# Kernel optimization log

Hardware: AMD Instinct MI355X
Metric: run time of the kernel (lower is better)

The kernel has to match this reference:

```python
import jax, jax.numpy as jnp
import numpy as np

NUM_DOTS = 100
IMG_SIZE = 4096


def setup_inputs() -> dict:
    key = jax.random.key(0)
    k1, k2, k3, k4 = jax.random.split(key, 4)
    adv_patch = jax.random.uniform(k1, (3, IMG_SIZE, IMG_SIZE), dtype=jnp.float32)
    centers = jax.random.uniform(k2, (NUM_DOTS, 2), dtype=jnp.float32)
    radii = jax.random.uniform(k3, (NUM_DOTS,), dtype=jnp.float32)
    colors = jax.random.uniform(k4, (NUM_DOTS, 3), dtype=jnp.float32)
    return {"adv_patch": adv_patch, "centers": centers, "radii": radii, "colors": colors}


def reference(adv_patch, centers, radii, colors):
    # Replicates PatchTrainer.forward: for each dot, draw a filled circle
    # (PIL ellipse with center (int(cx*S), int(cy*S)) and radius int(r*S/5))
    # and overwrite the three channels with the dot's color inside the circle.
    # Later dots overwrite earlier ones (sequential masked_fill_), so we scan.
    S = adv_patch.shape[-1]
    # int() truncation on non-negative values == floor
    xc = jnp.floor(centers[:, 0] * S)          # [N] horizontal center (image x)
    yc = jnp.floor(centers[:, 1] * S)          # [N] vertical center (image y)
    r = jnp.floor(radii * (S / 5.0))           # [N]
    xs = jnp.arange(S, dtype=adv_patch.dtype)  # columns (x)
    ys = jnp.arange(S, dtype=adv_patch.dtype)  # rows (y)

    def step(patch, dot):
        xci, yci, ri, col = dot
        # circle mask [S, S] indexed [y, x], matching ToTensor() layout
        d2 = (xs[None, :] - xci) ** 2 + (ys[:, None] - yci) ** 2
        mask = d2 <= ri * ri
        patch = jnp.where(mask[None, :, :], col[:, None, None], patch)
        return patch, None

    out, _ = jax.lax.scan(step, adv_patch, (xc, yc, r, colors))
    return out
```

## Files before the change

### kernel.cpp

```cpp
#include <hip/hip_runtime.h>


#define IMG  4096
#define ND   100
#define TW   256
#define TH   32
#define NBX  (IMG / TW)
#define NBY  (IMG / TH)

typedef float vfloat4 __attribute__((ext_vector_type(4)));

__global__ __launch_bounds__(256) void patch_dots_kernel(
    const float* __restrict__ patch,
    const float* __restrict__ centers,
    const float* __restrict__ radii,
    const float* __restrict__ colors,
    float* __restrict__ out)
{
    __shared__ float  s_xc[ND], s_yc[ND], s_r2[ND], s_col[ND];
    __shared__ int    s_list[ND];
    __shared__ unsigned long long s_mask[2];
    __shared__ int    s_cnt;

    const int bid = blockIdx.x;
    const int bx  = bid % NBX;
    const int by  = (bid / NBX) % NBY;
    const int z   = bid / (NBX * NBY);

    const int tx0 = bx * TW;
    const int ty0 = by * TH;
    const int t   = threadIdx.x;
    const int lane = t & 63;
    const int w    = t >> 6;

    const size_t plane = (size_t)z * IMG * IMG;

    int flag = 0;
    if (t < ND) {
        float xc = floorf(centers[2 * t]     * 4096.0f);
        float yc = floorf(centers[2 * t + 1] * 4096.0f);
        float r  = floorf(radii[t] * (4096.0f / 5.0f));
        float r2 = r * r;
        s_xc[t] = xc; s_yc[t] = yc; s_r2[t] = r2;
        s_col[t] = colors[3 * t + z];
        float cx = fminf(fmaxf(xc, (float)tx0), (float)(tx0 + TW - 1));
        float cy = fminf(fmaxf(yc, (float)ty0), (float)(ty0 + TH - 1));
        float dx = xc - cx, dy = yc - cy;
        flag = (dx * dx + dy * dy <= r2) ? 1 : 0;
    }
    if (t < 128) {
        unsigned long long m = __ballot(flag != 0);
        if (lane == 0) s_mask[w] = m;
    }
    __syncthreads();
    {
        const unsigned long long m0 = s_mask[0];
        if (flag) {
            const unsigned long long mw = s_mask[w];
            int pos = __popcll(mw & ((1ull << lane) - 1)) + (w ? __popcll(m0) : 0);
            s_list[pos] = t;
        }
        if (t == 0) s_cnt = __popcll(m0) + __popcll(s_mask[1]);
    }
    __syncthreads();
    const int cnt = s_cnt;

    const int x0   = tx0 + lane * 4;
    const float fx0 = (float)x0;
    const float fx1 = (float)(x0 + 1);
    const float fx2 = (float)(x0 + 2);
    const float fx3 = (float)(x0 + 3);

    for (int it = 0; it < TH / 4; ++it) {
        const int   y  = ty0 + it * 4 + w;
        const float fy = (float)y;

        int b0 = -1, b1 = -1, b2 = -1, b3 = -1;
        for (int k = cnt - 1; k >= 0; --k) {
            const int   i  = s_list[k];
            const float dy = fy - s_yc[i];
            const float t2 = s_r2[i] - dy * dy;
            if (t2 < 0.f) continue;
            const float xc = s_xc[i];
            const float dx0 = fx0 - xc;
            const float dx1 = fx1 - xc;
            const float dx2 = fx2 - xc;
            const float dx3 = fx3 - xc;
            if (b0 < 0 && dx0 * dx0 <= t2) b0 = i;
            if (b1 < 0 && dx1 * dx1 <= t2) b1 = i;
            if (b2 < 0 && dx2 * dx2 <= t2) b2 = i;
            if (b3 < 0 && dx3 * dx3 <= t2) b3 = i;
            if (__all((b0 | b1 | b2 | b3) >= 0)) break;
        }

        const size_t base = plane + (size_t)y * IMG + x0;

        float4 p = make_float4(0.f, 0.f, 0.f, 0.f);
        if ((b0 | b1 | b2 | b3) < 0) {
            const vfloat4 pv = __builtin_nontemporal_load((const vfloat4*)(patch + base));
            p = make_float4(pv.x, pv.y, pv.z, pv.w);
        }

        vfloat4 o;
        o.x = (b0 >= 0) ? s_col[b0] : p.x;
        o.y = (b1 >= 0) ? s_col[b1] : p.y;
        o.z = (b2 >= 0) ? s_col[b2] : p.z;
        o.w = (b3 >= 0) ? s_col[b3] : p.w;

        __builtin_nontemporal_store(o, (vfloat4*)(out + base));
    }
}

extern "C" void kernel_launch(void* const* d_in, const int* in_sizes, int n_in,
                              void* d_out, int out_size, void* d_ws, size_t ws_size,
                              hipStream_t stream) {
    const float* patch   = (const float*)d_in[0];
    const float* centers = (const float*)d_in[1];
    const float* radii   = (const float*)d_in[2];
    const float* colors  = (const float*)d_in[3];
    float* out = (float*)d_out;

    dim3 grid(NBX * NBY * 3);
    dim3 block(256);
    patch_dots_kernel<<<grid, block, 0, stream>>>(patch, centers, radii, colors, out);
}
```

Measured before the change: 304.4 us.

## Tile by full-width row strips instead of 256x32 blocks

Each block now processes 8 full image rows, a contiguous slab, instead of a 256x32 tile, and culls dots only by their vertical extent. This gives each block fully contiguous memory accesses and a simpler cull. The cost is that the per-block candidate list can be longer, since horizontal culling is gone, so the per-pixel search over dots may do more iterations where circles don't cover that x range.

```diff
diff --git a/kernel.cpp b/kernel.cpp
--- a/kernel.cpp
+++ b/kernel.cpp
@@ -1,12 +1,10 @@
 #include <hip/hip_runtime.h>
 
 
-#define IMG  4096
-#define ND   100
-#define TW   256
-#define TH   32
-#define NBX  (IMG / TW)
-#define NBY  (IMG / TH)
+#define IMG   4096
+#define ND    100
+#define ROWS  8
+#define NBB   (IMG / ROWS)
 
 typedef float vfloat4 __attribute__((ext_vector_type(4)));
 
@@ -23,17 +21,12 @@
     __shared__ int    s_cnt;
 
     const int bid = blockIdx.x;
-    const int bx  = bid % NBX;
-    const int by  = (bid / NBX) % NBY;
-    const int z   = bid / (NBX * NBY);
+    const int z   = bid / NBB;
+    const int ty0 = (bid % NBB) * ROWS;
 
-    const int tx0 = bx * TW;
-    const int ty0 = by * TH;
-    const int t   = threadIdx.x;
+    const int t    = threadIdx.x;
     const int lane = t & 63;
     const int w    = t >> 6;
-
-    const size_t plane = (size_t)z * IMG * IMG;
 
     int flag = 0;
     if (t < ND) {
@@ -43,10 +36,9 @@
         float r2 = r * r;
         s_xc[t] = xc; s_yc[t] = yc; s_r2[t] = r2;
         s_col[t] = colors[3 * t + z];
-        float cx = fminf(fmaxf(xc, (float)tx0), (float)(tx0 + TW - 1));
-        float cy = fminf(fmaxf(yc, (float)ty0), (float)(ty0 + TH - 1));
-        float dx = xc - cx, dy = yc - cy;
-        flag = (dx * dx + dy * dy <= r2) ? 1 : 0;
+        float cy = fminf(fmaxf(yc, (float)ty0), (float)(ty0 + ROWS - 1));
+        float dy = yc - cy;
+        flag = (dy * dy <= r2) ? 1 : 0;
     }
     if (t < 128) {
         unsigned long long m = __ballot(flag != 0);
@@ -65,15 +57,17 @@
     __syncthreads();
     const int cnt = s_cnt;
 
-    const int x0   = tx0 + lane * 4;
-    const float fx0 = (float)x0;
-    const float fx1 = (float)(x0 + 1);
-    const float fx2 = (float)(x0 + 2);
-    const float fx3 = (float)(x0 + 3);
+    const size_t slab = (size_t)z * IMG * IMG + (size_t)ty0 * IMG;
 
-    for (int it = 0; it < TH / 4; ++it) {
-        const int   y  = ty0 + it * 4 + w;
-        const float fy = (float)y;
+    for (int it = 0; it < ROWS * IMG / 1024; ++it) {
+        const int q   = it * 1024 + t * 4;
+        const int x0  = q & (IMG - 1);
+        const int yof = q >> 12;
+        const float fy  = (float)(ty0 + yof);
+        const float fx0 = (float)x0;
+        const float fx1 = (float)(x0 + 1);
+        const float fx2 = (float)(x0 + 2);
+        const float fx3 = (float)(x0 + 3);
 
         int b0 = -1, b1 = -1, b2 = -1, b3 = -1;
         for (int k = cnt - 1; k >= 0; --k) {
@@ -93,7 +87,7 @@
             if (__all((b0 | b1 | b2 | b3) >= 0)) break;
         }
 
-        const size_t base = plane + (size_t)y * IMG + x0;
+        const size_t base = slab + (size_t)q;
 
         float4 p = make_float4(0.f, 0.f, 0.f, 0.f);
         if ((b0 | b1 | b2 | b3) < 0) {
@@ -120,7 +114,7 @@
     const float* colors  = (const float*)d_in[3];
     float* out = (float*)d_out;
 
-    dim3 grid(NBX * NBY * 3);
+    dim3 grid(3 * NBB);
     dim3 block(256);
     patch_dots_kernel<<<grid, block, 0, stream>>>(patch, centers, radii, colors, out);
 }
```

Result: slower. 432.8 us (+42.2%).
